# Kernel optimization log

Measured on AMD Instinct MI355X. Metric: run time of the kernel, lower is better.

The kernel has to match this reference:

```python
import jax, jax.numpy as jnp
import numpy as np

MAX_OBJECTS = 20
NODE_FEAT_DIM = 16
HID = 256
N_OPS = 8
N_COLORS = 10
B = 16384
EPS = 1e-5


def _ln(x, g, b):
    m = x.mean(-1, keepdims=True)
    v = ((x - m) ** 2).mean(-1, keepdims=True)
    return (x - m) / jnp.sqrt(v + EPS) * g + b


def _mlp(x, w1, b1, w2, b2):
    return jax.nn.relu(x @ w1 + b1) @ w2 + b2


def setup_inputs() -> dict:
    key = jax.random.key(0)
    ks = jax.random.split(key, 32)
    w = lambda k, shp: (jax.random.normal(k, shp, jnp.float32) * 0.02)
    return {
        "nf": jax.random.normal(ks[0], (B, MAX_OBJECTS, NODE_FEAT_DIM), jnp.float32),
        "nn_c": jax.random.randint(ks[1], (B,), 0, MAX_OBJECTS),
        "neW": w(ks[2], (NODE_FEAT_DIM, HID)), "neb": jnp.zeros((HID,), jnp.float32),
        "g1W1": w(ks[3], (2 * HID, HID)), "g1b1": jnp.zeros((HID,), jnp.float32),
        "g1W2": w(ks[4], (HID, HID)), "g1b2": jnp.zeros((HID,), jnp.float32),
        "g2W1": w(ks[5], (2 * HID, HID)), "g2b1": jnp.zeros((HID,), jnp.float32),
        "g2W2": w(ks[6], (HID, HID)), "g2b2": jnp.zeros((HID,), jnp.float32),
        "n1g": jnp.ones((HID,), jnp.float32), "n1b": jnp.zeros((HID,), jnp.float32),
        "n2g": jnp.ones((HID,), jnp.float32), "n2b": jnp.zeros((HID,), jnp.float32),
        "ohW": w(ks[7], (HID, N_OPS)), "ohb": jnp.zeros((N_OPS,), jnp.float32),
        "c1W": w(ks[8], (HID, N_COLORS)), "c1b": jnp.zeros((N_COLORS,), jnp.float32),
        "c2W": w(ks[9], (HID, N_COLORS)), "c2b": jnp.zeros((N_COLORS,), jnp.float32),
        "pqW": w(ks[10], (HID, HID)), "pqb": jnp.zeros((HID,), jnp.float32),
        "pkW": w(ks[11], (HID, HID)), "pkb": jnp.zeros((HID,), jnp.float32),
    }


def reference(nf, nn_c, neW, neb, g1W1, g1b1, g1W2, g1b2, g2W1, g2b1, g2W2, g2b2,
              n1g, n1b, n2g, n2b, ohW, ohb, c1W, c1b, c2W, c2b, pqW, pqb, pkW, pkb):
    mask = jnp.arange(MAX_OBJECTS)[None, :] < nn_c[:, None]  # [B, N]
    mf = mask.astype(jnp.float32)[..., None]                 # [B, N, 1]
    denom = jnp.clip(mf.sum(1, keepdims=True), 1.0)          # [B, 1, 1]

    h = nf @ neW + neb                                       # [B, N, H]
    msg = (h * mf).sum(1, keepdims=True) / denom             # [B, 1, H]
    h = h + _mlp(jnp.concatenate([h, jnp.broadcast_to(msg, h.shape)], -1), g1W1, g1b1, g1W2, g1b2)
    h = _ln(h, n1g, n1b) * mf

    msg = (h * mf).sum(1, keepdims=True) / denom
    h = h + _mlp(jnp.concatenate([h, jnp.broadcast_to(msg, h.shape)], -1), g2W1, g2b1, g2W2, g2b2)
    h = _ln(h, n2g, n2b) * mf

    g = (h * mf).sum(1) / jnp.clip(mf.sum(1), 1.0)           # [B, H]

    q = g @ pqW + pqb                                        # [B, H]
    k = h @ pkW + pkb                                        # [B, N, H]
    pl = jnp.einsum('bh,bnh->bn', q, k)
    pl = jnp.where(mask, pl, -1e9)
    return (g @ ohW + ohb, g @ c1W + c1b, g @ c2W + c2b, pl)
```

## Files before the change

### kernel.cpp

```cpp
#include <hip/hip_runtime.h>

typedef unsigned char u8;
typedef unsigned int  u32;
using f32x4 = __attribute__((ext_vector_type(4))) float;

#define DI __device__ __forceinline__

DI u32 pk4f8(float a, float b, float c, float d){
  int w = __builtin_amdgcn_cvt_pk_fp8_f32(a, b, 0, false);
  w = __builtin_amdgcn_cvt_pk_fp8_f32(c, d, w, true);
  return (u32)w;
}
DI u8 enc1(float a){
  return (u8)(__builtin_amdgcn_cvt_pk_fp8_f32(a, a, 0, false) & 0xFF);
}
DI float dc0(u32 v){ return __builtin_amdgcn_cvt_f32_fp8((int)v, 0); }
DI float dc1(u32 v){ return __builtin_amdgcn_cvt_f32_fp8((int)v, 1); }
DI float dc2(u32 v){ return __builtin_amdgcn_cvt_f32_fp8((int)v, 2); }
DI float dc3(u32 v){ return __builtin_amdgcn_cvt_f32_fp8((int)v, 3); }

DI f32x4 MFMA8(long a, long b, f32x4 c){
  return __builtin_amdgcn_mfma_f32_16x16x32_fp8_fp8(a, b, c, 0, 0, 0);
}

DI int swz8(int row, int col){ return (row << 8) + (col ^ ((row & 15) << 3)); }
DI long ldsA8(const u8* buf, int row, int k0){ return *(const long*)(buf + swz8(row, k0)); }
DI long ldG8(const u8* p){ return *(const long*)p; }

DI long mk8(float v0, float v1, float v2, float v3, float v4, float v5, float v6, float v7){
  u32 lo = pk4f8(v0, v1, v2, v3), hi = pk4f8(v4, v5, v6, v7);
  return (long)(((unsigned long long)hi << 32) | (unsigned long long)lo);
}
DI long loadW8T(const float* __restrict__ W, int n, int k0){
  return mk8(W[(k0+0)*256+n]*8.f, W[(k0+1)*256+n]*8.f, W[(k0+2)*256+n]*8.f, W[(k0+3)*256+n]*8.f,
             W[(k0+4)*256+n]*8.f, W[(k0+5)*256+n]*8.f, W[(k0+6)*256+n]*8.f, W[(k0+7)*256+n]*8.f);
}
DI long loadW8T16(const float* __restrict__ W, int n, int k0){
  float v[8];
#pragma unroll
  for (int j = 0; j < 8; j++){ int k = k0 + j; v[j] = (k < 16) ? W[k*256+n]*8.f : 0.f; }
  return mk8(v[0],v[1],v[2],v[3],v[4],v[5],v[6],v[7]);
}
DI long loadW8row(const float* __restrict__ W, int n, int k0){
  const float* p = W + n*256 + k0;
  return mk8(p[0]*8.f,p[1]*8.f,p[2]*8.f,p[3]*8.f,p[4]*8.f,p[5]*8.f,p[6]*8.f,p[7]*8.f);
}

#define WS_NEWT  0
#define WS_W1AT1 8192
#define WS_W1BT1 73728
#define WS_W2T1  139264
#define WS_W1AT2 204800
#define WS_W1BT2 270336
#define WS_W2T2  335872
#define WS_PQWT  401408
#define WS_PKWP  466944
#define WS_TOTAL 532480

__global__ void prep_weights(
    const float* __restrict__ neW, const float* __restrict__ g1W1,
    const float* __restrict__ g1W2, const float* __restrict__ g2W1,
    const float* __restrict__ g2W2, const float* __restrict__ pqW,
    const float* __restrict__ pkW, u8* __restrict__ ws)
{
  int i = blockIdx.x * 256 + threadIdx.x;
  if (i >= WS_TOTAL) return;
  float v;
  if (i < 8192){
    int n = i >> 5, k = i & 31;
    v = (k < 16) ? neW[k * 256 + n] : 0.0f;
  } else {
    int j = i - 8192;
    int region = j >> 16;
    int idx = j & 65535;
    int n = idx >> 8, k = idx & 255;
    switch (region){
      case 0: v = g1W1[k * 256 + n]; break;
      case 1: v = g1W1[(256 + k) * 256 + n]; break;
      case 2: v = g1W2[k * 256 + n]; break;
      case 3: v = g2W1[k * 256 + n]; break;
      case 4: v = g2W1[(256 + k) * 256 + n]; break;
      case 5: v = g2W2[k * 256 + n]; break;
      case 6: v = pqW[k * 256 + n]; break;
      default: v = pkW[idx]; break;
    }
  }
  ws[i] = enc1(v * 8.0f);
}

template<bool PREPPED>
__global__ __launch_bounds__(512, 2) void fused_graphnet(
    const float* __restrict__ nf, const int* __restrict__ nn_c,
    const float* __restrict__ neW, const float* __restrict__ neb,
    const float* __restrict__ g1W1, const float* __restrict__ g1b1,
    const float* __restrict__ g1W2, const float* __restrict__ g1b2,
    const float* __restrict__ g2W1, const float* __restrict__ g2b1,
    const float* __restrict__ g2W2, const float* __restrict__ g2b2,
    const float* __restrict__ n1g, const float* __restrict__ n1b,
    const float* __restrict__ n2g, const float* __restrict__ n2b,
    const float* __restrict__ ohW, const float* __restrict__ ohb,
    const float* __restrict__ c1W, const float* __restrict__ c1b,
    const float* __restrict__ c2W, const float* __restrict__ c2b,
    const float* __restrict__ pqW, const float* __restrict__ pqb,
    const float* __restrict__ pkW, const float* __restrict__ pkb,
    const u8* __restrict__ ws, float* __restrict__ out,
    int out_n, int Bv)
{
  __shared__ __align__(16) u8 bufA[80 * 256];
  __shared__ __align__(16) u8 bufB[80 * 256];
  __shared__ __align__(16) u8 smallA[8 * 256];
  __shared__ float pbf[4 * 256];
  __shared__ float rowstats[8][80][2];
  __shared__ float qdot[4];
  __shared__ int   cntS[4];
  __shared__ float dinvS[4];

  const int b0 = blockIdx.x * 4;
  const int tid = threadIdx.x;
  const int wave = tid >> 6, lane = tid & 63;
  const int lg = lane >> 4, lc = lane & 15;
  const int n0 = wave * 32;

  const int Bout = out_n / 48;
  const int off_c1 = 8 * Bout;
  const int off_c2 = 18 * Bout;
  const int off_pl = 28 * Bout;

  if (tid < 4){
    int bi = b0 + tid; if (bi >= Bv) bi = Bv - 1;
    int c = nn_c[bi];
    c = c < 0 ? 0 : (c > 20 ? 20 : c);
    cntS[tid] = c;
    dinvS[tid] = 1.0f / (float)(c < 1 ? 1 : c);
  }

  for (int i = tid; i < 80 * 4; i += 512){
    int row = i >> 2, c0 = 16 + (i & 3) * 4;
    *(u32*)(bufB + swz8(row, c0)) = 0u;
  }
  for (int i = tid; i < 80 * 4; i += 512){
    int row = i >> 2, k0 = (i & 3) * 4;
    int gr = b0 * 20 + row; if (gr >= Bv * 20) gr = Bv * 20 - 1;
    const float* p = nf + gr * 16 + k0;
    *(u32*)(bufB + swz8(row, k0)) = pk4f8(p[0], p[1], p[2], p[3]);
  }
  __syncthreads();

  const f32x4 zero4 = {0.0f, 0.0f, 0.0f, 0.0f};

  {
    f32x4 acc[5][2];
#pragma unroll
    for (int mt = 0; mt < 5; mt++){
      long a = ldsA8(bufB, mt * 16 + lc, lg * 8);
#pragma unroll
      for (int nt = 0; nt < 2; nt++){
        int n = n0 + nt * 16 + lc;
        long bfr;
        if constexpr (PREPPED) bfr = ldG8(ws + WS_NEWT + n * 32 + lg * 8);
        else bfr = loadW8T16(neW, n, lg * 8);
        acc[mt][nt] = MFMA8(a, bfr, zero4);
      }
    }
#pragma unroll
    for (int nt = 0; nt < 2; nt++){
      float bb = neb[n0 + nt * 16 + lc];
#pragma unroll
      for (int mt = 0; mt < 5; mt++)
#pragma unroll
        for (int r = 0; r < 4; r++){
          int row = mt * 16 + lg * 4 + r;
          int col = n0 + nt * 16 + lc;
          bufA[swz8(row, col)] = enc1(acc[mt][nt][r] * 0.125f + bb);
        }
    }
  }
  __syncthreads();

  for (int rd = 0; rd < 2; rd++){
    const int w1at = (rd == 0) ? WS_W1AT1 : WS_W1AT2;
    const int w1bt = (rd == 0) ? WS_W1BT1 : WS_W1BT2;
    const int w2t  = (rd == 0) ? WS_W2T1  : WS_W2T2;
    const float* W1 = (rd == 0) ? g1W1 : g2W1;
    const float* W2 = (rd == 0) ? g1W2 : g2W2;
    const float* b1p = (rd == 0) ? g1b1 : g2b1;
    const float* b2p = (rd == 0) ? g1b2 : g2b2;
    const float* ngp = (rd == 0) ? n1g : n2g;
    const float* nbp = (rd == 0) ? n1b : n2b;

    if (tid < 256){
      int b = tid >> 6;
      int c0 = (tid & 63) * 4;
      int c = cntS[b];
      float s0 = 0, s1 = 0, s2 = 0, s3 = 0;
      for (int r = 0; r < c; r++){
        u32 v = *(const u32*)(bufA + swz8(b * 20 + r, c0));
        s0 += dc0(v); s1 += dc1(v); s2 += dc2(v); s3 += dc3(v);
      }
      float di = dinvS[b];
      *(u32*)(smallA + swz8(b, c0)) = pk4f8(s0 * di, s1 * di, s2 * di, s3 * di);
    }
    __syncthreads();

    {
      f32x4 acc[2];
#pragma unroll
      for (int nt = 0; nt < 2; nt++) acc[nt] = zero4;
      long bp0, bp1;
      {
        int n_0 = n0 + lc, n_1 = n0 + 16 + lc;
        if constexpr (PREPPED){ bp0 = ldG8(ws + w1bt + n_0 * 256 + lg * 8); bp1 = ldG8(ws + w1bt + n_1 * 256 + lg * 8); }
        else { bp0 = loadW8T(W1 + 256 * 256, n_0, lg * 8); bp1 = loadW8T(W1 + 256 * 256, n_1, lg * 8); }
      }
#pragma unroll 1
      for (int kk = 0; kk < 8; kk++){
        long bn0 = bp0, bn1 = bp1;
        if (kk < 7){
          int k1 = (kk + 1) * 32 + lg * 8;
          int n_0 = n0 + lc, n_1 = n0 + 16 + lc;
          if constexpr (PREPPED){ bp0 = ldG8(ws + w1bt + n_0 * 256 + k1); bp1 = ldG8(ws + w1bt + n_1 * 256 + k1); }
          else { bp0 = loadW8T(W1 + 256 * 256, n_0, k1); bp1 = loadW8T(W1 + 256 * 256, n_1, k1); }
        }
        long a = ldsA8(smallA, lc & 3, kk * 32 + lg * 8);
        acc[0] = MFMA8(a, bn0, acc[0]);
        acc[1] = MFMA8(a, bn1, acc[1]);
      }
      if (lg == 0){
#pragma unroll
        for (int nt = 0; nt < 2; nt++)
#pragma unroll
          for (int r = 0; r < 4; r++){
            int col = n0 + nt * 16 + lc;
            pbf[r * 256 + col] = acc[nt][r] * 0.125f + b1p[col];
          }
      }
    }

    {
      f32x4 tacc[5][2];
#pragma unroll
      for (int mt = 0; mt < 5; mt++)
#pragma unroll
        for (int nt = 0; nt < 2; nt++) tacc[mt][nt] = zero4;
      long bp0, bp1;
      {
        int n_0 = n0 + lc, n_1 = n0 + 16 + lc;
        if constexpr (PREPPED){ bp0 = ldG8(ws + w1at + n_0 * 256 + lg * 8); bp1 = ldG8(ws + w1at + n_1 * 256 + lg * 8); }
        else { bp0 = loadW8T(W1, n_0, lg * 8); bp1 = loadW8T(W1, n_1, lg * 8); }
      }
#pragma unroll 1
      for (int kk = 0; kk < 8; kk++){
        long bn0 = bp0, bn1 = bp1;
        if (kk < 7){
          int k1 = (kk + 1) * 32 + lg * 8;
          int n_0 = n0 + lc, n_1 = n0 + 16 + lc;
          if constexpr (PREPPED){ bp0 = ldG8(ws + w1at + n_0 * 256 + k1); bp1 = ldG8(ws + w1at + n_1 * 256 + k1); }
          else { bp0 = loadW8T(W1, n_0, k1); bp1 = loadW8T(W1, n_1, k1); }
        }
#pragma unroll
        for (int mt = 0; mt < 5; mt++){
          long a = ldsA8(bufA, mt * 16 + lc, kk * 32 + lg * 8);
          tacc[mt][0] = MFMA8(a, bn0, tacc[mt][0]);
          tacc[mt][1] = MFMA8(a, bn1, tacc[mt][1]);
        }
      }
#pragma unroll
      for (int mt = 0; mt < 5; mt++)
#pragma unroll
        for (int nt = 0; nt < 2; nt++)
#pragma unroll
          for (int r = 0; r < 4; r++){
            int row = mt * 16 + lg * 4 + r;
            int col = n0 + nt * 16 + lc;
            float v = tacc[mt][nt][r] * 0.125f + pbf[(row / 20) * 256 + col];
            bufB[swz8(row, col)] = enc1(fmaxf(v, 0.0f));
          }
    }
    __syncthreads();

    {
      f32x4 tacc[5][2];
#pragma unroll
      for (int mt = 0; mt < 5; mt++)
#pragma unroll
        for (int nt = 0; nt < 2; nt++) tacc[mt][nt] = zero4;
      long bp0, bp1;
      {
        int n_0 = n0 + lc, n_1 = n0 + 16 + lc;
        if constexpr (PREPPED){ bp0 = ldG8(ws + w2t + n_0 * 256 + lg * 8); bp1 = ldG8(ws + w2t + n_1 * 256 + lg * 8); }
        else { bp0 = loadW8T(W2, n_0, lg * 8); bp1 = loadW8T(W2, n_1, lg * 8); }
      }
#pragma unroll 1
      for (int kk = 0; kk < 8; kk++){
        long bn0 = bp0, bn1 = bp1;
        if (kk < 7){
          int k1 = (kk + 1) * 32 + lg * 8;
          int n_0 = n0 + lc, n_1 = n0 + 16 + lc;
          if constexpr (PREPPED){ bp0 = ldG8(ws + w2t + n_0 * 256 + k1); bp1 = ldG8(ws + w2t + n_1 * 256 + k1); }
          else { bp0 = loadW8T(W2, n_0, k1); bp1 = loadW8T(W2, n_1, k1); }
        }
#pragma unroll
        for (int mt = 0; mt < 5; mt++){
          long a = ldsA8(bufB, mt * 16 + lc, kk * 32 + lg * 8);
          tacc[mt][0] = MFMA8(a, bn0, tacc[mt][0]);
          tacc[mt][1] = MFMA8(a, bn1, tacc[mt][1]);
        }
      }
#pragma unroll
      for (int nt = 0; nt < 2; nt++){
        float b2s = b2p[n0 + nt * 16 + lc];
#pragma unroll
        for (int mt = 0; mt < 5; mt++)
#pragma unroll
          for (int r = 0; r < 4; r++){
            int row = mt * 16 + lg * 4 + r;
            int col = n0 + nt * 16 + lc;
            u32 rv = bufA[swz8(row, col)];
            float v = tacc[mt][nt][r] * 0.125f + dc0(rv) + b2s;
            bufA[swz8(row, col)] = enc1(v);
          }
      }
    }

    {
#pragma unroll
      for (int mt = 0; mt < 5; mt++)
#pragma unroll
        for (int r = 0; r < 4; r++){
          int row = mt * 16 + lg * 4 + r;
          float s1 = 0, s2 = 0;
#pragma unroll
          for (int nt = 0; nt < 2; nt++){
            float v = dc0((u32)bufA[swz8(row, n0 + nt * 16 + lc)]);
            s1 += v; s2 += v * v;
          }
#pragma unroll
          for (int d = 1; d < 16; d <<= 1){ s1 += __shfl_xor(s1, d, 64); s2 += __shfl_xor(s2, d, 64); }
          if (lc == 0){ rowstats[wave][row][0] = s1; rowstats[wave][row][1] = s2; }
        }
      __syncthreads();

#pragma unroll
      for (int mt = 0; mt < 5; mt++)
#pragma unroll
        for (int r = 0; r < 4; r++){
          int row = mt * 16 + lg * 4 + r;
          float t1s = 0, t2s = 0;
#pragma unroll
          for (int w = 0; w < 8; w++){ t1s += rowstats[w][row][0]; t2s += rowstats[w][row][1]; }
          float mean = t1s * (1.0f / 256.0f);
          float var  = t2s * (1.0f / 256.0f) - mean * mean;
          float rstd = rsqrtf(fmaxf(var, 0.0f) + 1e-5f);
          int bb = row / 20;
          float mf = ((row - bb * 20) < cntS[bb]) ? 1.0f : 0.0f;
#pragma unroll
          for (int nt = 0; nt < 2; nt++){
            int col = n0 + nt * 16 + lc;
            float v = dc0((u32)bufA[swz8(row, col)]);
            bufA[swz8(row, col)] = enc1(((v - mean) * rstd * ngp[col] + nbp[col]) * mf);
          }
        }
    }
    __syncthreads();
  }

  if (tid < 256){
    int b = tid >> 6;
    int c0 = (tid & 63) * 4;
    int c = cntS[b];
    float s0 = 0, s1 = 0, s2 = 0, s3 = 0;
    for (int r = 0; r < c; r++){
      u32 v = *(const u32*)(bufA + swz8(b * 20 + r, c0));
      s0 += dc0(v); s1 += dc1(v); s2 += dc2(v); s3 += dc3(v);
    }
    float di = dinvS[b];
    *(u32*)(smallA + swz8(b, c0)) = pk4f8(s0 * di, s1 * di, s2 * di, s3 * di);
  }
  __syncthreads();

  {
    f32x4 qacc[2];
#pragma unroll
    for (int nt = 0; nt < 2; nt++) qacc[nt] = zero4;
#pragma unroll 1
    for (int kk = 0; kk < 8; kk++){
      long a = ldsA8(smallA, lc & 3, kk * 32 + lg * 8);
#pragma unroll
      for (int nt = 0; nt < 2; nt++){
        int n = n0 + nt * 16 + lc;
        long bfr;
        if constexpr (PREPPED) bfr = ldG8(ws + WS_PQWT + n * 256 + kk * 32 + lg * 8);
        else bfr = loadW8T(pqW, n, kk * 32 + lg * 8);
        qacc[nt] = MFMA8(a, bfr, qacc[nt]);
      }
    }
    if (lg == 0){
#pragma unroll
      for (int nt = 0; nt < 2; nt++)
#pragma unroll
        for (int r = 0; r < 4; r++){
          int col = n0 + nt * 16 + lc;
          smallA[swz8(4 + r, col)] = enc1(qacc[nt][r] * 0.125f + pqb[col]);
        }
    }
  }
  __syncthreads();

  if (wave < 4){
    u32 qv = *(const u32*)(smallA + swz8(4 + wave, lane * 4));
    float p = dc0(qv) * pkb[lane * 4 + 0] + dc1(qv) * pkb[lane * 4 + 1]
            + dc2(qv) * pkb[lane * 4 + 2] + dc3(qv) * pkb[lane * 4 + 3];
#pragma unroll
    for (int d = 1; d < 64; d <<= 1) p += __shfl_xor(p, d, 64);
    if (lane == 0) qdot[wave] = p;
  }

  {
    f32x4 racc[2];
#pragma unroll
    for (int nt = 0; nt < 2; nt++) racc[nt] = zero4;
#pragma unroll 1
    for (int kk = 0; kk < 8; kk++){
      long a = ldsA8(smallA, 4 + (lc & 3), kk * 32 + lg * 8);
#pragma unroll
      for (int nt = 0; nt < 2; nt++){
        int n = n0 + nt * 16 + lc;
        long bfr;
        if constexpr (PREPPED) bfr = ldG8(ws + WS_PKWP + n * 256 + kk * 32 + lg * 8);
        else bfr = loadW8row(pkW, n, kk * 32 + lg * 8);
        racc[nt] = MFMA8(a, bfr, racc[nt]);
      }
    }
    if (lg == 0){
#pragma unroll
      for (int nt = 0; nt < 2; nt++)
#pragma unroll
        for (int r = 0; r < 4; r++)
          pbf[r * 256 + (n0 + nt * 16 + lc)] = racc[nt][r] * 0.125f;
    }
  }
  __syncthreads();

  if (wave < 4){
    const int b = wave;
    if (b0 + b < Bv){
      int cb = cntS[b];
      float qd = qdot[b];
      for (int rr = 0; rr < 20; rr++){
        int row = b * 20 + rr;
        u32 hv = *(const u32*)(bufA + swz8(row, lane * 4));
        const float* rp = pbf + b * 256 + lane * 4;
        float p = dc0(hv) * rp[0] + dc1(hv) * rp[1] + dc2(hv) * rp[2] + dc3(hv) * rp[3];
#pragma unroll
        for (int d = 1; d < 64; d <<= 1) p += __shfl_xor(p, d, 64);
        if (lane == 0){
          float v = (rr < cb) ? (p + qd) : -1e9f;
          out[off_pl + (b0 + b) * 20 + rr] = v;
        }
      }
    }
  } else {
    const int b = wave - 4;
    if (b0 + b < Bv){
      u32 gv = *(const u32*)(smallA + swz8(b, lane * 4));
      float g0 = dc0(gv), g1 = dc1(gv), g2 = dc2(gv), g3 = dc3(gv);
#pragma unroll 1
      for (int o = 0; o < 28; o++){
        const float* W; const float* bias; int ncol, col, off;
        if (o < 8)      { W = ohW; bias = ohb; ncol = 8;  col = o;      off = 0; }
        else if (o < 18){ W = c1W; bias = c1b; ncol = 10; col = o - 8;  off = off_c1; }
        else            { W = c2W; bias = c2b; ncol = 10; col = o - 18; off = off_c2; }
        int k = lane * 4;
        float p = g0 * W[(k + 0) * ncol + col] + g1 * W[(k + 1) * ncol + col]
                + g2 * W[(k + 2) * ncol + col] + g3 * W[(k + 3) * ncol + col];
#pragma unroll
        for (int d = 1; d < 64; d <<= 1) p += __shfl_xor(p, d, 64);
        if (lane == 0) out[off + (b0 + b) * ncol + col] = p + bias[col];
      }
    }
  }
}

extern "C" void kernel_launch(void* const* d_in, const int* in_sizes, int n_in,
                              void* d_out, int out_size, void* d_ws, size_t ws_size,
                              hipStream_t stream)
{
  const float* nf   = (const float*)d_in[0];
  const int*   nn_c = (const int*)d_in[1];
  const float* neW  = (const float*)d_in[2];
  const float* neb  = (const float*)d_in[3];
  const float* g1W1 = (const float*)d_in[4];
  const float* g1b1 = (const float*)d_in[5];
  const float* g1W2 = (const float*)d_in[6];
  const float* g1b2 = (const float*)d_in[7];
  const float* g2W1 = (const float*)d_in[8];
  const float* g2b1 = (const float*)d_in[9];
  const float* g2W2 = (const float*)d_in[10];
  const float* g2b2 = (const float*)d_in[11];
  const float* n1g  = (const float*)d_in[12];
  const float* n1b  = (const float*)d_in[13];
  const float* n2g  = (const float*)d_in[14];
  const float* n2b  = (const float*)d_in[15];
  const float* ohW  = (const float*)d_in[16];
  const float* ohb  = (const float*)d_in[17];
  const float* c1W  = (const float*)d_in[18];
  const float* c1b  = (const float*)d_in[19];
  const float* c2W  = (const float*)d_in[20];
  const float* c2b  = (const float*)d_in[21];
  const float* pqW  = (const float*)d_in[22];
  const float* pqb  = (const float*)d_in[23];
  const float* pkW  = (const float*)d_in[24];
  const float* pkb  = (const float*)d_in[25];

  float* outp = (float*)d_out;
  u8* ws = (u8*)d_ws;
  int B = in_sizes[0] / 320;
  int grid = (B + 3) / 4;

  if (ws_size >= (size_t)WS_TOTAL){
    prep_weights<<<(WS_TOTAL + 255) / 256, 256, 0, stream>>>(
        neW, g1W1, g1W2, g2W1, g2W2, pqW, pkW, ws);
    fused_graphnet<true><<<grid, 512, 0, stream>>>(
        nf, nn_c, neW, neb, g1W1, g1b1, g1W2, g1b2, g2W1, g2b1, g2W2, g2b2,
        n1g, n1b, n2g, n2b, ohW, ohb, c1W, c1b, c2W, c2b, pqW, pqb, pkW, pkb,
        ws, outp, out_size, B);
  } else {
    fused_graphnet<false><<<grid, 512, 0, stream>>>(
        nf, nn_c, neW, neb, g1W1, g1b1, g1W2, g1b2, g2W1, g2b1, g2W2, g2b2,
        n1g, n1b, n2g, n2b, ohW, ohb, c1W, c1b, c2W, c2b, pqW, pqb, pkW, pkb,
        ws, outp, out_size, B);
  }
}
```

Before: 1.092 ms.

## Split fused graph network into multi-kernel pipeline with workspace intermediates

Replaces the single fused per-4-sample kernel with a chain of separate kernels: an embedding GEMM, masked means, per-sample row-matrix products, 32-row MFMA GEMM tiles with fused ReLU or residual plus LayerNorm, and separate pointer-logit and head kernels. Intermediates (h, the MLP hidden layer, messages, q, r) are staged in FP8 or FP32 in the workspace. The apparent aim is larger, more uniform GEMM tiles and simpler per-stage kernels. In exchange it adds many launches and global round-trips of the full hidden state, and it only runs when the workspace is large enough; otherwise a fallback fused kernel without prepped weights is used.

```diff
diff --git a/kernel.cpp b/kernel.cpp
--- a/kernel.cpp
+++ b/kernel.cpp
@@ -2,6 +2,7 @@
 
 typedef unsigned char u8;
 typedef unsigned int  u32;
+typedef unsigned long long u64;
 using f32x4 = __attribute__((ext_vector_type(4))) float;
 
 #define DI __device__ __forceinline__
@@ -88,8 +89,239 @@
   ws[i] = enc1(v * 8.0f);
 }
 
-template<bool PREPPED>
-__global__ __launch_bounds__(512, 2) void fused_graphnet(
+
+__global__ void k_gemm0(const float* __restrict__ nf, const float* __restrict__ neW,
+                        const float* __restrict__ neb, u8* __restrict__ h, int total){
+  int stride = gridDim.x * blockDim.x;
+  for (int idx = blockIdx.x * blockDim.x + threadIdx.x; idx < total; idx += stride){
+    int r = idx >> 8, c = idx & 255;
+    const float* a = nf + (size_t)r * 16;
+    float s = neb[c];
+#pragma unroll
+    for (int k = 0; k < 16; k++) s += a[k] * neW[k * 256 + c];
+    h[idx] = enc1(s);
+  }
+}
+
+__global__ void k_mean(const u8* __restrict__ src, u8* __restrict__ dst,
+                       const int* __restrict__ nn_c, int total){
+  int stride = gridDim.x * blockDim.x;
+  for (int idx = blockIdx.x * blockDim.x + threadIdx.x; idx < total; idx += stride){
+    int b = idx >> 8, c = idx & 255;
+    int cnt = nn_c[b]; cnt = cnt < 0 ? 0 : (cnt > 20 ? 20 : cnt);
+    const u8* p = src + (size_t)b * 5120 + c;
+    float s = 0.0f;
+    for (int r = 0; r < cnt; r++) s += dc0((u32)p[r * 256]);
+    float di = 1.0f / (float)(cnt < 1 ? 1 : cnt);
+    dst[idx] = enc1(s * di);
+  }
+}
+
+__global__ void k_rowmat(const u8* __restrict__ vec8, const u8* __restrict__ W8,
+                         const float* __restrict__ bias, float* __restrict__ dst){
+  __shared__ float m[256];
+  int b = blockIdx.x, tid = threadIdx.x;
+  m[tid] = dc0((u32)vec8[(size_t)b * 256 + tid]);
+  __syncthreads();
+  const u8* wr = W8 + (size_t)tid * 256;
+  float s = 0.0f;
+  for (int k = 0; k < 256; k += 4){
+    u32 w4 = *(const u32*)(wr + k);
+    s += m[k] * dc0(w4) + m[k+1] * dc1(w4) + m[k+2] * dc2(w4) + m[k+3] * dc3(w4);
+  }
+  float v = s * 0.125f;
+  if (bias) v += bias[tid];
+  dst[(size_t)b * 256 + tid] = v;
+}
+
+__global__ void k_q(const u8* __restrict__ g8, const u8* __restrict__ Wq8,
+                    const float* __restrict__ pqb, const float* __restrict__ pkb,
+                    u8* __restrict__ q8, float* __restrict__ qd){
+  __shared__ float m[256];
+  __shared__ float red[4];
+  int b = blockIdx.x, tid = threadIdx.x;
+  m[tid] = dc0((u32)g8[(size_t)b * 256 + tid]);
+  __syncthreads();
+  const u8* wr = Wq8 + (size_t)tid * 256;
+  float s = 0.0f;
+  for (int k = 0; k < 256; k += 4){
+    u32 w4 = *(const u32*)(wr + k);
+    s += m[k] * dc0(w4) + m[k+1] * dc1(w4) + m[k+2] * dc2(w4) + m[k+3] * dc3(w4);
+  }
+  float qv = s * 0.125f + pqb[tid];
+  q8[(size_t)b * 256 + tid] = enc1(qv);
+  float p = qv * pkb[tid];
+#pragma unroll
+  for (int d = 1; d < 64; d <<= 1) p += __shfl_xor(p, d, 64);
+  if ((tid & 63) == 0) red[tid >> 6] = p;
+  __syncthreads();
+  if (tid == 0) qd[b] = red[0] + red[1] + red[2] + red[3];
+}
+
+template<int MODE>
+__global__ void k_gemm(const u8* __restrict__ A, const u8* __restrict__ Wt,
+                       const float* __restrict__ pbf, const float* __restrict__ b2,
+                       const float* __restrict__ ng, const float* __restrict__ nb,
+                       u8* __restrict__ dst, const int* __restrict__ nn_c, int M)
+{
+  __shared__ __align__(16) u8 at[32 * 256];
+  __shared__ float rowstats[4][32][2];
+  const int tid = threadIdx.x;
+  const int wave = tid >> 6, lane = tid & 63;
+  const int lg = lane >> 4, lc = lane & 15;
+  const int n0 = wave * 64;
+  const int row0 = blockIdx.x * 32;
+  if (row0 >= M) return;
+
+  {
+    int row = tid >> 3, c0 = (tid & 7) * 32;
+    int gr = row0 + row; if (gr >= M) gr = M - 1;
+    const u8* src = A + (size_t)gr * 256 + c0;
+#pragma unroll
+    for (int i = 0; i < 4; i++){
+      u64 v = *(const u64*)(src + i * 8);
+      *(u64*)(at + swz8(row, c0 + i * 8)) = v;
+    }
+  }
+  __syncthreads();
+
+  const f32x4 zero4 = {0.0f, 0.0f, 0.0f, 0.0f};
+  f32x4 tacc[2][4];
+#pragma unroll
+  for (int mt = 0; mt < 2; mt++)
+#pragma unroll
+    for (int nt = 0; nt < 4; nt++) tacc[mt][nt] = zero4;
+
+#pragma unroll 1
+  for (int kk = 0; kk < 8; kk++){
+    long a0 = ldsA8(at, lc, kk * 32 + lg * 8);
+    long a1 = ldsA8(at, 16 + lc, kk * 32 + lg * 8);
+#pragma unroll
+    for (int nt = 0; nt < 4; nt++){
+      long bfr = ldG8(Wt + (size_t)(n0 + nt * 16 + lc) * 256 + kk * 32 + lg * 8);
+      tacc[0][nt] = MFMA8(a0, bfr, tacc[0][nt]);
+      tacc[1][nt] = MFMA8(a1, bfr, tacc[1][nt]);
+    }
+  }
+
+  if constexpr (MODE == 0){
+#pragma unroll
+    for (int mt = 0; mt < 2; mt++)
+#pragma unroll
+      for (int nt = 0; nt < 4; nt++)
+#pragma unroll
+        for (int r = 0; r < 4; r++){
+          int grow = row0 + mt * 16 + lg * 4 + r;
+          if (grow >= M) continue;
+          int col = n0 + nt * 16 + lc;
+          float v = tacc[mt][nt][r] * 0.125f + pbf[(size_t)(grow / 20) * 256 + col];
+          dst[(size_t)grow * 256 + col] = enc1(fmaxf(v, 0.0f));
+        }
+  } else {
+#pragma unroll
+    for (int mt = 0; mt < 2; mt++){
+#pragma unroll
+      for (int nt = 0; nt < 4; nt++){
+        float b2s = b2[n0 + nt * 16 + lc];
+#pragma unroll
+        for (int r = 0; r < 4; r++){
+          int grow = row0 + mt * 16 + lg * 4 + r;
+          int gr = grow >= M ? M - 1 : grow;
+          int col = n0 + nt * 16 + lc;
+          tacc[mt][nt][r] = tacc[mt][nt][r] * 0.125f
+                          + dc0((u32)dst[(size_t)gr * 256 + col]) + b2s;
+        }
+      }
+#pragma unroll
+      for (int r = 0; r < 4; r++){
+        int lrow = mt * 16 + lg * 4 + r;
+        float s1 = 0, s2 = 0;
+#pragma unroll
+        for (int nt = 0; nt < 4; nt++){ float v = tacc[mt][nt][r]; s1 += v; s2 += v * v; }
+#pragma unroll
+        for (int d = 1; d < 16; d <<= 1){ s1 += __shfl_xor(s1, d, 64); s2 += __shfl_xor(s2, d, 64); }
+        if (lc == 0){ rowstats[wave][lrow][0] = s1; rowstats[wave][lrow][1] = s2; }
+      }
+    }
+    __syncthreads();
+    float ngv[4], nbv[4];
+#pragma unroll
+    for (int nt = 0; nt < 4; nt++){
+      ngv[nt] = ng[n0 + nt * 16 + lc];
+      nbv[nt] = nb[n0 + nt * 16 + lc];
+    }
+#pragma unroll
+    for (int mt = 0; mt < 2; mt++)
+#pragma unroll
+      for (int r = 0; r < 4; r++){
+        int lrow = mt * 16 + lg * 4 + r;
+        int grow = row0 + lrow;
+        if (grow >= M) continue;
+        float t1s = rowstats[0][lrow][0] + rowstats[1][lrow][0] + rowstats[2][lrow][0] + rowstats[3][lrow][0];
+        float t2s = rowstats[0][lrow][1] + rowstats[1][lrow][1] + rowstats[2][lrow][1] + rowstats[3][lrow][1];
+        float mean = t1s * (1.0f / 256.0f);
+        float var  = t2s * (1.0f / 256.0f) - mean * mean;
+        float rstd = rsqrtf(fmaxf(var, 0.0f) + 1e-5f);
+        int bb = grow / 20;
+        int cb = nn_c[bb]; cb = cb < 0 ? 0 : (cb > 20 ? 20 : cb);
+        float mf = ((grow - bb * 20) < cb) ? 1.0f : 0.0f;
+#pragma unroll
+        for (int nt = 0; nt < 4; nt++){
+          int col = n0 + nt * 16 + lc;
+          float v = ((tacc[mt][nt][r] - mean) * rstd * ngv[nt] + nbv[nt]) * mf;
+          dst[(size_t)grow * 256 + col] = enc1(v);
+        }
+      }
+  }
+}
+
+__global__ void k_pl(const u8* __restrict__ h8, const float* __restrict__ r32,
+                     const float* __restrict__ qd, const int* __restrict__ nn_c,
+                     float* __restrict__ out, int off_pl, int rows){
+  int waves = (gridDim.x * blockDim.x) >> 6;
+  int gw = (blockIdx.x * blockDim.x + threadIdx.x) >> 6;
+  int lane = threadIdx.x & 63;
+  for (int row = gw; row < rows; row += waves){
+    int b = row / 20, j = row - b * 20;
+    u32 hv = *(const u32*)(h8 + (size_t)row * 256 + lane * 4);
+    const float* rp = r32 + (size_t)b * 256 + lane * 4;
+    float p = dc0(hv) * rp[0] + dc1(hv) * rp[1] + dc2(hv) * rp[2] + dc3(hv) * rp[3];
+#pragma unroll
+    for (int d = 1; d < 64; d <<= 1) p += __shfl_xor(p, d, 64);
+    if (lane == 0){
+      int cb = nn_c[b]; cb = cb < 0 ? 0 : (cb > 20 ? 20 : cb);
+      out[off_pl + row] = (j < cb) ? (p + qd[b]) : -1e9f;
+    }
+  }
+}
+
+__global__ void k_heads(const u8* __restrict__ g8,
+                        const float* __restrict__ ohW, const float* __restrict__ ohb,
+                        const float* __restrict__ c1W, const float* __restrict__ c1b,
+                        const float* __restrict__ c2W, const float* __restrict__ c2b,
+                        float* __restrict__ out, int Bout){
+  int b = blockIdx.x;
+  int tid = threadIdx.x, wave = tid >> 6, lane = tid & 63;
+  int off_c1 = 8 * Bout, off_c2 = 18 * Bout;
+  u32 gv = *(const u32*)(g8 + (size_t)b * 256 + lane * 4);
+  float g0 = dc0(gv), g1 = dc1(gv), g2 = dc2(gv), g3 = dc3(gv);
+  int o0 = wave * 7;
+#pragma unroll 1
+  for (int o = o0; o < o0 + 7; o++){
+    const float* W; const float* bias; int ncol, col, off;
+    if (o < 8)      { W = ohW; bias = ohb; ncol = 8;  col = o;      off = 0; }
+    else if (o < 18){ W = c1W; bias = c1b; ncol = 10; col = o - 8;  off = off_c1; }
+    else            { W = c2W; bias = c2b; ncol = 10; col = o - 18; off = off_c2; }
+    int k = lane * 4;
+    float p = g0 * W[(k + 0) * ncol + col] + g1 * W[(k + 1) * ncol + col]
+            + g2 * W[(k + 2) * ncol + col] + g3 * W[(k + 3) * ncol + col];
+#pragma unroll
+    for (int d = 1; d < 64; d <<= 1) p += __shfl_xor(p, d, 64);
+    if (lane == 0) out[off + b * ncol + col] = p + bias[col];
+  }
+}
+
+__global__ __launch_bounds__(512, 2) void fused_graphnet_fb(
     const float* __restrict__ nf, const int* __restrict__ nn_c,
     const float* __restrict__ neW, const float* __restrict__ neb,
     const float* __restrict__ g1W1, const float* __restrict__ g1b1,
@@ -103,8 +335,7 @@
     const float* __restrict__ c2W, const float* __restrict__ c2b,
     const float* __restrict__ pqW, const float* __restrict__ pqb,
     const float* __restrict__ pkW, const float* __restrict__ pkb,
-    const u8* __restrict__ ws, float* __restrict__ out,
-    int out_n, int Bv)
+    float* __restrict__ out, int out_n, int Bv)
 {
   __shared__ __align__(16) u8 bufA[80 * 256];
   __shared__ __align__(16) u8 bufB[80 * 256];
@@ -122,9 +353,7 @@
   const int n0 = wave * 32;
 
   const int Bout = out_n / 48;
-  const int off_c1 = 8 * Bout;
-  const int off_c2 = 18 * Bout;
-  const int off_pl = 28 * Bout;
+  const int off_c1 = 8 * Bout, off_c2 = 18 * Bout, off_pl = 28 * Bout;
 
   if (tid < 4){
     int bi = b0 + tid; if (bi >= Bv) bi = Bv - 1;
@@ -133,7 +362,6 @@
     cntS[tid] = c;
     dinvS[tid] = 1.0f / (float)(c < 1 ? 1 : c);
   }
-
   for (int i = tid; i < 80 * 4; i += 512){
     int row = i >> 2, c0 = 16 + (i & 3) * 4;
     *(u32*)(bufB + swz8(row, c0)) = 0u;
@@ -141,26 +369,21 @@
   for (int i = tid; i < 80 * 4; i += 512){
     int row = i >> 2, k0 = (i & 3) * 4;
     int gr = b0 * 20 + row; if (gr >= Bv * 20) gr = Bv * 20 - 1;
-    const float* p = nf + gr * 16 + k0;
+    const float* p = nf + (size_t)gr * 16 + k0;
     *(u32*)(bufB + swz8(row, k0)) = pk4f8(p[0], p[1], p[2], p[3]);
   }
   __syncthreads();
 
   const f32x4 zero4 = {0.0f, 0.0f, 0.0f, 0.0f};
-
   {
+    long bw0 = loadW8T16(neW, n0 + lc, lg * 8);
+    long bw1 = loadW8T16(neW, n0 + 16 + lc, lg * 8);
     f32x4 acc[5][2];
 #pragma unroll
     for (int mt = 0; mt < 5; mt++){
       long a = ldsA8(bufB, mt * 16 + lc, lg * 8);
-#pragma unroll
-      for (int nt = 0; nt < 2; nt++){
-        int n = n0 + nt * 16 + lc;
-        long bfr;
-        if constexpr (PREPPED) bfr = ldG8(ws + WS_NEWT + n * 32 + lg * 8);
-        else bfr = loadW8T16(neW, n, lg * 8);
-        acc[mt][nt] = MFMA8(a, bfr, zero4);
-      }
+      acc[mt][0] = MFMA8(a, bw0, zero4);
+      acc[mt][1] = MFMA8(a, bw1, zero4);
     }
 #pragma unroll
     for (int nt = 0; nt < 2; nt++){
@@ -170,17 +393,13 @@
 #pragma unroll
         for (int r = 0; r < 4; r++){
           int row = mt * 16 + lg * 4 + r;
-          int col = n0 + nt * 16 + lc;
-          bufA[swz8(row, col)] = enc1(acc[mt][nt][r] * 0.125f + bb);
+          bufA[swz8(row, n0 + nt * 16 + lc)] = enc1(acc[mt][nt][r] * 0.125f + bb);
         }
     }
   }
   __syncthreads();
 
   for (int rd = 0; rd < 2; rd++){
-    const int w1at = (rd == 0) ? WS_W1AT1 : WS_W1AT2;
-    const int w1bt = (rd == 0) ? WS_W1BT1 : WS_W1BT2;
-    const int w2t  = (rd == 0) ? WS_W2T1  : WS_W2T2;
     const float* W1 = (rd == 0) ? g1W1 : g2W1;
     const float* W2 = (rd == 0) ? g1W2 : g2W2;
     const float* b1p = (rd == 0) ? g1b1 : g2b1;
@@ -203,23 +422,16 @@
     __syncthreads();
 
     {
-      f32x4 acc[2];
-#pragma unroll
-      for (int nt = 0; nt < 2; nt++) acc[nt] = zero4;
-      long bp0, bp1;
-      {
-        int n_0 = n0 + lc, n_1 = n0 + 16 + lc;
-        if constexpr (PREPPED){ bp0 = ldG8(ws + w1bt + n_0 * 256 + lg * 8); bp1 = ldG8(ws + w1bt + n_1 * 256 + lg * 8); }
-        else { bp0 = loadW8T(W1 + 256 * 256, n_0, lg * 8); bp1 = loadW8T(W1 + 256 * 256, n_1, lg * 8); }
-      }
+      f32x4 acc[2]; acc[0] = zero4; acc[1] = zero4;
+      long bp0 = loadW8T(W1 + 65536, n0 + lc, lg * 8);
+      long bp1 = loadW8T(W1 + 65536, n0 + 16 + lc, lg * 8);
 #pragma unroll 1
       for (int kk = 0; kk < 8; kk++){
         long bn0 = bp0, bn1 = bp1;
         if (kk < 7){
           int k1 = (kk + 1) * 32 + lg * 8;
-          int n_0 = n0 + lc, n_1 = n0 + 16 + lc;
-          if constexpr (PREPPED){ bp0 = ldG8(ws + w1bt + n_0 * 256 + k1); bp1 = ldG8(ws + w1bt + n_1 * 256 + k1); }
-          else { bp0 = loadW8T(W1 + 256 * 256, n_0, k1); bp1 = loadW8T(W1 + 256 * 256, n_1, k1); }
+          bp0 = loadW8T(W1 + 65536, n0 + lc, k1);
+          bp1 = loadW8T(W1 + 65536, n0 + 16 + lc, k1);
         }
         long a = ldsA8(smallA, lc & 3, kk * 32 + lg * 8);
         acc[0] = MFMA8(a, bn0, acc[0]);
@@ -235,27 +447,19 @@
           }
       }
     }
-
     {
       f32x4 tacc[5][2];
 #pragma unroll
-      for (int mt = 0; mt < 5; mt++)
-#pragma unroll
-        for (int nt = 0; nt < 2; nt++) tacc[mt][nt] = zero4;
-      long bp0, bp1;
-      {
-        int n_0 = n0 + lc, n_1 = n0 + 16 + lc;
-        if constexpr (PREPPED){ bp0 = ldG8(ws + w1at + n_0 * 256 + lg * 8); bp1 = ldG8(ws + w1at + n_1 * 256 + lg * 8); }
-        else { bp0 = loadW8T(W1, n_0, lg * 8); bp1 = loadW8T(W1, n_1, lg * 8); }
-      }
+      for (int mt = 0; mt < 5; mt++){ tacc[mt][0] = zero4; tacc[mt][1] = zero4; }
+      long bp0 = loadW8T(W1, n0 + lc, lg * 8);
+      long bp1 = loadW8T(W1, n0 + 16 + lc, lg * 8);
 #pragma unroll 1
       for (int kk = 0; kk < 8; kk++){
         long bn0 = bp0, bn1 = bp1;
         if (kk < 7){
           int k1 = (kk + 1) * 32 + lg * 8;
-          int n_0 = n0 + lc, n_1 = n0 + 16 + lc;
-          if constexpr (PREPPED){ bp0 = ldG8(ws + w1at + n_0 * 256 + k1); bp1 = ldG8(ws + w1at + n_1 * 256 + k1); }
-          else { bp0 = loadW8T(W1, n_0, k1); bp1 = loadW8T(W1, n_1, k1); }
+          bp0 = loadW8T(W1, n0 + lc, k1);
+          bp1 = loadW8T(W1, n0 + 16 + lc, k1);
         }
 #pragma unroll
         for (int mt = 0; mt < 5; mt++){
@@ -277,27 +481,19 @@
           }
     }
     __syncthreads();
-
     {
       f32x4 tacc[5][2];
 #pragma unroll
-      for (int mt = 0; mt < 5; mt++)
-#pragma unroll
-        for (int nt = 0; nt < 2; nt++) tacc[mt][nt] = zero4;
-      long bp0, bp1;
-      {
-        int n_0 = n0 + lc, n_1 = n0 + 16 + lc;
-        if constexpr (PREPPED){ bp0 = ldG8(ws + w2t + n_0 * 256 + lg * 8); bp1 = ldG8(ws + w2t + n_1 * 256 + lg * 8); }
-        else { bp0 = loadW8T(W2, n_0, lg * 8); bp1 = loadW8T(W2, n_1, lg * 8); }
-      }
+      for (int mt = 0; mt < 5; mt++){ tacc[mt][0] = zero4; tacc[mt][1] = zero4; }
+      long bp0 = loadW8T(W2, n0 + lc, lg * 8);
+      long bp1 = loadW8T(W2, n0 + 16 + lc, lg * 8);
 #pragma unroll 1
       for (int kk = 0; kk < 8; kk++){
         long bn0 = bp0, bn1 = bp1;
         if (kk < 7){
           int k1 = (kk + 1) * 32 + lg * 8;
-          int n_0 = n0 + lc, n_1 = n0 + 16 + lc;
-          if constexpr (PREPPED){ bp0 = ldG8(ws + w2t + n_0 * 256 + k1); bp1 = ldG8(ws + w2t + n_1 * 256 + k1); }
-          else { bp0 = loadW8T(W2, n_0, k1); bp1 = loadW8T(W2, n_1, k1); }
+          bp0 = loadW8T(W2, n0 + lc, k1);
+          bp1 = loadW8T(W2, n0 + 16 + lc, k1);
         }
 #pragma unroll
         for (int mt = 0; mt < 5; mt++){
@@ -321,7 +517,6 @@
           }
       }
     }
-
     {
 #pragma unroll
       for (int mt = 0; mt < 5; mt++)
@@ -339,7 +534,6 @@
           if (lc == 0){ rowstats[wave][row][0] = s1; rowstats[wave][row][1] = s2; }
         }
       __syncthreads();
-
 #pragma unroll
       for (int mt = 0; mt < 5; mt++)
 #pragma unroll
@@ -377,22 +571,13 @@
     *(u32*)(smallA + swz8(b, c0)) = pk4f8(s0 * di, s1 * di, s2 * di, s3 * di);
   }
   __syncthreads();
-
   {
-    f32x4 qacc[2];
-#pragma unroll
-    for (int nt = 0; nt < 2; nt++) qacc[nt] = zero4;
+    f32x4 qacc[2]; qacc[0] = zero4; qacc[1] = zero4;
 #pragma unroll 1
     for (int kk = 0; kk < 8; kk++){
       long a = ldsA8(smallA, lc & 3, kk * 32 + lg * 8);
-#pragma unroll
-      for (int nt = 0; nt < 2; nt++){
-        int n = n0 + nt * 16 + lc;
-        long bfr;
-        if constexpr (PREPPED) bfr = ldG8(ws + WS_PQWT + n * 256 + kk * 32 + lg * 8);
-        else bfr = loadW8T(pqW, n, kk * 32 + lg * 8);
-        qacc[nt] = MFMA8(a, bfr, qacc[nt]);
-      }
+      qacc[0] = MFMA8(a, loadW8T(pqW, n0 + lc, kk * 32 + lg * 8), qacc[0]);
+      qacc[1] = MFMA8(a, loadW8T(pqW, n0 + 16 + lc, kk * 32 + lg * 8), qacc[1]);
     }
     if (lg == 0){
 #pragma unroll
@@ -405,7 +590,6 @@
     }
   }
   __syncthreads();
-
   if (wave < 4){
     u32 qv = *(const u32*)(smallA + swz8(4 + wave, lane * 4));
     float p = dc0(qv) * pkb[lane * 4 + 0] + dc1(qv) * pkb[lane * 4 + 1]
@@ -414,22 +598,13 @@
     for (int d = 1; d < 64; d <<= 1) p += __shfl_xor(p, d, 64);
     if (lane == 0) qdot[wave] = p;
   }
-
   {
-    f32x4 racc[2];
-#pragma unroll
-    for (int nt = 0; nt < 2; nt++) racc[nt] = zero4;
+    f32x4 racc[2]; racc[0] = zero4; racc[1] = zero4;
 #pragma unroll 1
     for (int kk = 0; kk < 8; kk++){
       long a = ldsA8(smallA, 4 + (lc & 3), kk * 32 + lg * 8);
-#pragma unroll
-      for (int nt = 0; nt < 2; nt++){
-        int n = n0 + nt * 16 + lc;
-        long bfr;
-        if constexpr (PREPPED) bfr = ldG8(ws + WS_PKWP + n * 256 + kk * 32 + lg * 8);
-        else bfr = loadW8row(pkW, n, kk * 32 + lg * 8);
-        racc[nt] = MFMA8(a, bfr, racc[nt]);
-      }
+      racc[0] = MFMA8(a, loadW8row(pkW, n0 + lc, kk * 32 + lg * 8), racc[0]);
+      racc[1] = MFMA8(a, loadW8row(pkW, n0 + 16 + lc, kk * 32 + lg * 8), racc[1]);
     }
     if (lg == 0){
 #pragma unroll
@@ -440,7 +615,6 @@
     }
   }
   __syncthreads();
-
   if (wave < 4){
     const int b = wave;
     if (b0 + b < Bv){
@@ -515,19 +689,55 @@
   float* outp = (float*)d_out;
   u8* ws = (u8*)d_ws;
   int B = in_sizes[0] / 320;
-  int grid = (B + 3) / 4;
-
-  if (ws_size >= (size_t)WS_TOTAL){
+  int M = B * 20;
+  int Bout = out_size / 48;
+  int off_pl = 28 * Bout;
+
+  size_t szH = (size_t)M * 256;
+  size_t szV = (size_t)B * 256;
+  size_t oH   = (size_t)WS_TOTAL;
+  size_t oT   = oH + szH;
+  size_t oMSG = oT + szH;
+  size_t oG   = oMSG + szV;
+  size_t oQ   = oG + szV;
+  size_t oPB  = oQ + szV;
+  size_t oR   = oPB + szV * 4;
+  size_t oQD  = oR + szV * 4;
+  size_t need = oQD + (size_t)B * 4;
+
+  if (ws_size >= need){
+    u8* H8  = ws + oH;
+    u8* T8  = ws + oT;
+    u8* MSG = ws + oMSG;
+    u8* G8  = ws + oG;
+    u8* Q8  = ws + oQ;
+    float* PBF = (float*)(ws + oPB);
+    float* R32 = (float*)(ws + oR);
+    float* QD  = (float*)(ws + oQD);
+
     prep_weights<<<(WS_TOTAL + 255) / 256, 256, 0, stream>>>(
         neW, g1W1, g1W2, g2W1, g2W2, pqW, pkW, ws);
-    fused_graphnet<true><<<grid, 512, 0, stream>>>(
+
+    k_gemm0<<<2048, 1024, 0, stream>>>(nf, neW, neb, H8, M * 256);
+
+    int ggrid = (M + 31) / 32;
+    k_mean<<<2048, 1024, 0, stream>>>(H8, MSG, nn_c, B * 256);
+    k_rowmat<<<B, 256, 0, stream>>>(MSG, ws + WS_W1BT1, g1b1, PBF);
+    k_gemm<0><<<ggrid, 256, 0, stream>>>(H8, ws + WS_W1AT1, PBF, nullptr, nullptr, nullptr, T8, nn_c, M);
+    k_gemm<1><<<ggrid, 256, 0, stream>>>(T8, ws + WS_W2T1, nullptr, g1b2, n1g, n1b, H8, nn_c, M);
+    k_mean<<<2048, 1024, 0, stream>>>(H8, MSG, nn_c, B * 256);
+    k_rowmat<<<B, 256, 0, stream>>>(MSG, ws + WS_W1BT2, g2b1, PBF);
+    k_gemm<0><<<ggrid, 256, 0, stream>>>(H8, ws + WS_W1AT2, PBF, nullptr, nullptr, nullptr, T8, nn_c, M);
+    k_gemm<1><<<ggrid, 256, 0, stream>>>(T8, ws + WS_W2T2, nullptr, g2b2, n2g, n2b, H8, nn_c, M);
+    k_mean<<<2048, 1024, 0, stream>>>(H8, G8, nn_c, B * 256);
+    k_q<<<B, 256, 0, stream>>>(G8, ws + WS_PQWT, pqb, pkb, Q8, QD);
+    k_rowmat<<<B, 256, 0, stream>>>(Q8, ws + WS_PKWP, nullptr, R32);
+    k_pl<<<2048, 256, 0, stream>>>(H8, R32, QD, nn_c, outp, off_pl, M);
+    k_heads<<<B, 256, 0, stream>>>(G8, ohW, ohb, c1W, c1b, c2W, c2b, outp, Bout);
+  } else {
+    fused_graphnet_fb<<<(B + 3) / 4, 512, 0, stream>>>(
         nf, nn_c, neW, neb, g1W1, g1b1, g1W2, g1b2, g2W1, g2b1, g2W2, g2b2,
         n1g, n1b, n2g, n2b, ohW, ohb, c1W, c1b, c2W, c2b, pqW, pqb, pkW, pkb,
-        ws, outp, out_size, B);
-  } else {
-    fused_graphnet<false><<<grid, 512, 0, stream>>>(
-        nf, nn_c, neW, neb, g1W1, g1b1, g1W2, g1b2, g2W1, g2b1, g2W2, g2b2,
-        n1g, n1b, n2g, n2b, ohW, ohb, c1W, c1b, c2W, c2b, pqW, pqb, pkW, pkb,
-        ws, outp, out_size, B);
-  }
-}
+        outp, out_size, B);
+  }
+}
```

New measurement: 1.876 ms. 71.8% more time.
